# Kernel optimization log

Hardware: AMD Instinct MI355X
Metric: run time of the kernel (lower is better)

The kernel has to match this reference:

```python
import jax, jax.numpy as jnp
import numpy as np

N = 320          # number of valid codes in the batch
D = 128          # spatial dims; embeddings are (N, D+1) Lorentz points
MIN_DIST = 0.1
MARGIN = 0.1
WEIGHT = 0.1


def setup_inputs() -> dict:
    key = jax.random.key(0)
    k1, k2 = jax.random.split(key)
    # Valid hyperboloid points: x0 = sqrt(1 + ||x_spatial||^2)
    sp = 0.5 * jax.random.normal(k1, (N, D), dtype=jnp.float32)
    x0 = jnp.sqrt(1.0 + jnp.sum(sp * sp, axis=-1, keepdims=True))
    embeddings = jnp.concatenate([x0, sp], axis=-1)  # (N, D+1)
    # Symmetric nonnegative tree-distance matrix with zero diagonal
    td = jax.random.uniform(k2, (N, N), dtype=jnp.float32) * 8.0
    td = 0.5 * (td + td.T)
    td = td * (1.0 - jnp.eye(N, dtype=jnp.float32))
    return {"embeddings": embeddings, "tree_distances": td}


def _lorentz_pairwise(x):
    # Lorentz (hyperboloid) distance: d = arccosh(-<x,y>_L),
    # <x,y>_L = -x0*y0 + x_sp . y_sp
    t = x[:, :1]
    sp = x[:, 1:]
    inner = sp @ sp.T - t @ t.T  # (N, N) Minkowski inner product
    return jnp.arccosh(jnp.clip(-inner, 1.0 + 1e-7, None))


def reference(embeddings, tree_distances):
    emb = _lorentz_pairwise(embeddings)      # (N, N) embedding distances
    gt = tree_distances                       # (N, N) ground-truth distances
    n = gt.shape[0]
    # valid[a, j]: gt distance >= min_distance and j != a
    valid = (gt >= MIN_DIST) & (~jnp.eye(n, dtype=bool))
    # axes: (anchor a, j, k).  s > 0 iff gt[a,j] < gt[a,k]
    s = jnp.sign(gt[:, None, :] - gt[:, :, None])          # (N, N, N)
    diff = emb[:, :, None] - emb[:, None, :]                # e_j - e_k
    viol = jax.nn.relu(s * diff + MARGIN)                   # (N, N, N)
    tri = jnp.triu(jnp.ones((n, n), dtype=bool), 1)[None]   # j < k
    mask = valid[:, :, None] & valid[:, None, :] & tri & (s != 0.0)
    total = jnp.sum(jnp.where(mask, viol, 0.0))
    count = jnp.sum((viol > 0.0) & mask).astype(jnp.float32)
    return WEIGHT * jnp.where(count > 0.0, total / jnp.maximum(count, 1.0), 0.0)
```

## Files before the change

kernel.cpp:

```cpp
#include <hip/hip_runtime.h>
#include <math.h>

#define NN 320
#define DFULL 129
#define MIN_DIST_F 0.1f
#define MARGIN_F 0.1f
#define WEIGHT_F 0.1f
#define KG 5
#define JC 4
#define JLEN 80
#define NPART (NN*KG*JC)
#define NTILE 20
#define NTRI (NTILE*(NTILE+1)/2)

__device__ __forceinline__ int tri_off(int a) { return a * NTILE - (a * (a - 1)) / 2; }

__global__ __launch_bounds__(256) void lorentz_kernel(const float* __restrict__ E,
                                                      const float* __restrict__ gt,
                                                      float* __restrict__ embp) {
    const int t = blockIdx.x;
    float fa = (2.0f * NTILE + 1.0f - sqrtf((2.0f*NTILE+1.0f)*(2.0f*NTILE+1.0f) - 8.0f * (float)t)) * 0.5f;
    int a = (int)fa;
    if (a > 0 && tri_off(a) > t) --a;
    if (tri_off(a + 1) <= t) ++a;
    const int b = a + (t - tri_off(a));
    const int i0 = a * 16, j0 = b * 16;

    __shared__ float As[16][DFULL];
    __shared__ float Bs[16][DFULL];
    for (int q = threadIdx.x; q < 16 * DFULL; q += 256) {
        int r = q / DFULL, c = q - r * DFULL;
        As[r][c] = E[(i0 + r) * DFULL + c];
        Bs[r][c] = E[(j0 + r) * DFULL + c];
    }
    __syncthreads();
    const int ti = threadIdx.x & 15;
    const int tj = threadIdx.x >> 4;
    const int i = i0 + tj, j = j0 + ti;
    float tt = As[tj][0] * Bs[ti][0];
    float ss = 0.0f;
    #pragma unroll
    for (int d = 1; d < DFULL; ++d) ss = fmaf(As[tj][d], Bs[ti][d], ss);
    float x = fmaxf(tt - ss, 1.0f + 1e-7f);
    float e = acoshf(x);
    float g = gt[i * NN + j];
    float ep = (g >= MIN_DIST_F && i != j) ? e : __builtin_nanf("");
    embp[i * NN + j] = ep;
    embp[j * NN + i] = ep;
}

__global__ __launch_bounds__(64) void loss_kernel(const float* __restrict__ embp,
                                                  const float* __restrict__ gt,
                                                  float2* __restrict__ partial) {
    const int i    = blockIdx.x;
    const int kg   = blockIdx.y;
    const int jc   = blockIdx.z;
    const int lane = threadIdx.x;
    const int k    = kg * 64 + lane;

    const float* __restrict__ erow = embp + i * NN;
    const float* __restrict__ grow = gt   + i * NN;
    const float ek = erow[k];
    const float gk = grow[k];

    float tot = 0.0f, cnt = 0.0f;
    const int j0 = jc * JLEN;
    #pragma unroll
    for (int jb = 0; jb < JLEN; jb += 4) {
        const float4 e4 = *reinterpret_cast<const float4*>(erow + j0 + jb);
        const float4 g4 = *reinterpret_cast<const float4*>(grow + j0 + jb);
        {   float d = gk - g4.x; float v = fmaf(copysignf(1.0f, d), e4.x - ek, MARGIN_F);
            bool p = v > 0.0f; tot += p ? v : 0.0f; cnt += p ? 1.0f : 0.0f; }
        {   float d = gk - g4.y; float v = fmaf(copysignf(1.0f, d), e4.y - ek, MARGIN_F);
            bool p = v > 0.0f; tot += p ? v : 0.0f; cnt += p ? 1.0f : 0.0f; }
        {   float d = gk - g4.z; float v = fmaf(copysignf(1.0f, d), e4.z - ek, MARGIN_F);
            bool p = v > 0.0f; tot += p ? v : 0.0f; cnt += p ? 1.0f : 0.0f; }
        {   float d = gk - g4.w; float v = fmaf(copysignf(1.0f, d), e4.w - ek, MARGIN_F);
            bool p = v > 0.0f; tot += p ? v : 0.0f; cnt += p ? 1.0f : 0.0f; }
    }
    const bool self = (ek == ek) && (k >= j0) && (k < j0 + JLEN);
    if (self) { tot -= MARGIN_F; cnt -= 1.0f; }

    for (int off = 32; off > 0; off >>= 1) {
        tot += __shfl_down(tot, off, 64);
        cnt += __shfl_down(cnt, off, 64);
    }
    if (lane == 0) partial[(jc * KG + kg) * NN + i] = make_float2(tot, cnt);
}

__global__ __launch_bounds__(NN) void finalize_kernel(const float2* __restrict__ partial,
                                                      float* __restrict__ out) {
    const int t = threadIdx.x;
    float T = 0.0f, C = 0.0f;
    #pragma unroll
    for (int q = 0; q < NPART / NN; ++q) {
        float2 p = partial[q * NN + t];
        T += p.x; C += p.y;
    }
    for (int off = 32; off > 0; off >>= 1) {
        T += __shfl_down(T, off, 64);
        C += __shfl_down(C, off, 64);
    }
    __shared__ float wt[5], wc[5];
    const int lane = t & 63, wid = t >> 6;
    if (lane == 0) { wt[wid] = T; wc[wid] = C; }
    __syncthreads();
    if (t == 0) {
        float Tt = 0.0f, Ct = 0.0f;
        #pragma unroll
        for (int w = 0; w < 5; w++) { Tt += wt[w]; Ct += wc[w]; }
        out[0] = (Ct > 0.0f) ? WEIGHT_F * Tt / Ct : 0.0f;
    }
}

extern "C" void kernel_launch(void* const* d_in, const int* in_sizes, int n_in,
                              void* d_out, int out_size, void* d_ws, size_t ws_size,
                              hipStream_t stream) {
    const float* E  = (const float*)d_in[0];
    const float* gt = (const float*)d_in[1];
    float* out = (float*)d_out;
    float2* partial = (float2*)d_ws;
    float*  embp = (float*)((char*)d_ws + NPART * 8);

    lorentz_kernel<<<NTRI, 256, 0, stream>>>(E, gt, embp);
    dim3 g2(NN, KG, JC);
    loss_kernel<<<g2, 64, 0, stream>>>(embp, gt, partial);
    finalize_kernel<<<1, NN, 0, stream>>>(partial, out);
}
```

Baseline: 21.16 us.

## Fuse finalize into loss kernel via last-block atomic gate reduction

Removes the separate finalize launch. The loss kernel is now a persistent grid of 256 blocks that loop over the work units, and the last block to finish, found with an atomic counter reset by the lorentz kernel, reduces the per-block partials. Counts are accumulated as integers through ballot and popcount, and each block combines its waves' partials in shared memory. This saves one kernel launch and the many tiny 64-thread blocks, at the cost of atomics, fences and a serial tail in the last block.

Result: slower. 29.67 us (+40.2%).

```diff
diff --git a/kernel.cpp b/kernel.cpp
--- a/kernel.cpp
+++ b/kernel.cpp
@@ -6,18 +6,21 @@
 #define MIN_DIST_F 0.1f
 #define MARGIN_F 0.1f
 #define WEIGHT_F 0.1f
-#define KG 5
-#define JC 4
-#define JLEN 80
-#define NPART (NN*KG*JC)
 #define NTILE 20
 #define NTRI (NTILE*(NTILE+1)/2)
+#define JLEN 80
+#define NUNITS 6400
+#define LBLK 256
+#define LTHR 512
+#define NWAVE (LBLK*(LTHR/64))
 
 __device__ __forceinline__ int tri_off(int a) { return a * NTILE - (a * (a - 1)) / 2; }
 
 __global__ __launch_bounds__(256) void lorentz_kernel(const float* __restrict__ E,
                                                       const float* __restrict__ gt,
-                                                      float* __restrict__ embp) {
+                                                      float* __restrict__ embp,
+                                                      unsigned* __restrict__ gate) {
+    if (blockIdx.x == 0 && threadIdx.x == 0) *gate = 0u;
     const int t = blockIdx.x;
     float fa = (2.0f * NTILE + 1.0f - sqrtf((2.0f*NTILE+1.0f)*(2.0f*NTILE+1.0f) - 8.0f * (float)t)) * 0.5f;
     int a = (int)fa;
@@ -49,67 +52,89 @@
     embp[j * NN + i] = ep;
 }
 
-__global__ __launch_bounds__(64) void loss_kernel(const float* __restrict__ embp,
-                                                  const float* __restrict__ gt,
-                                                  float2* __restrict__ partial) {
-    const int i    = blockIdx.x;
-    const int kg   = blockIdx.y;
-    const int jc   = blockIdx.z;
-    const int lane = threadIdx.x;
-    const int k    = kg * 64 + lane;
+__global__ __launch_bounds__(LTHR) void loss_kernel(const float* __restrict__ embp,
+                                                    const float* __restrict__ gt,
+                                                    unsigned* __restrict__ gate,
+                                                    float* __restrict__ pT,
+                                                    float* __restrict__ pC,
+                                                    float* __restrict__ out) {
+    const int lane = threadIdx.x & 63;
+    const int wid  = threadIdx.x >> 6;
+    const int gw   = blockIdx.x * (LTHR / 64) + wid;
 
-    const float* __restrict__ erow = embp + i * NN;
-    const float* __restrict__ grow = gt   + i * NN;
-    const float ek = erow[k];
-    const float gk = grow[k];
+    float tot = 0.0f;
+    int   cnt = 0;
 
-    float tot = 0.0f, cnt = 0.0f;
-    const int j0 = jc * JLEN;
-    #pragma unroll
-    for (int jb = 0; jb < JLEN; jb += 4) {
-        const float4 e4 = *reinterpret_cast<const float4*>(erow + j0 + jb);
-        const float4 g4 = *reinterpret_cast<const float4*>(grow + j0 + jb);
-        {   float d = gk - g4.x; float v = fmaf(copysignf(1.0f, d), e4.x - ek, MARGIN_F);
-            bool p = v > 0.0f; tot += p ? v : 0.0f; cnt += p ? 1.0f : 0.0f; }
-        {   float d = gk - g4.y; float v = fmaf(copysignf(1.0f, d), e4.y - ek, MARGIN_F);
-            bool p = v > 0.0f; tot += p ? v : 0.0f; cnt += p ? 1.0f : 0.0f; }
-        {   float d = gk - g4.z; float v = fmaf(copysignf(1.0f, d), e4.z - ek, MARGIN_F);
-            bool p = v > 0.0f; tot += p ? v : 0.0f; cnt += p ? 1.0f : 0.0f; }
-        {   float d = gk - g4.w; float v = fmaf(copysignf(1.0f, d), e4.w - ek, MARGIN_F);
-            bool p = v > 0.0f; tot += p ? v : 0.0f; cnt += p ? 1.0f : 0.0f; }
+    for (int unit = gw; unit < NUNITS; unit += NWAVE) {
+        const int i  = unit / 20;
+        const int r  = unit - i * 20;
+        const int kg = r >> 2;
+        const int jc = r & 3;
+        const int k  = (kg << 6) + lane;
+        const float* __restrict__ erow = embp + i * NN;
+        const float* __restrict__ grow = gt   + i * NN;
+        const float ek = erow[k];
+        const float gk = grow[k];
+        const int j0 = jc * JLEN;
+
+        #pragma unroll 4
+        for (int jb = 0; jb < JLEN; jb += 4) {
+            const float4 e4 = *reinterpret_cast<const float4*>(erow + j0 + jb);
+            const float4 g4 = *reinterpret_cast<const float4*>(grow + j0 + jb);
+            {   float d = gk - g4.x; float v = fmaf(copysignf(1.0f, d), e4.x - ek, MARGIN_F);
+                bool p = v > 0.0f; tot += p ? v : 0.0f; cnt += (int)__popcll(__ballot(p)); }
+            {   float d = gk - g4.y; float v = fmaf(copysignf(1.0f, d), e4.y - ek, MARGIN_F);
+                bool p = v > 0.0f; tot += p ? v : 0.0f; cnt += (int)__popcll(__ballot(p)); }
+            {   float d = gk - g4.z; float v = fmaf(copysignf(1.0f, d), e4.z - ek, MARGIN_F);
+                bool p = v > 0.0f; tot += p ? v : 0.0f; cnt += (int)__popcll(__ballot(p)); }
+            {   float d = gk - g4.w; float v = fmaf(copysignf(1.0f, d), e4.w - ek, MARGIN_F);
+                bool p = v > 0.0f; tot += p ? v : 0.0f; cnt += (int)__popcll(__ballot(p)); }
+        }
+        bool self = (ek == ek) && (k >= j0) && (k < j0 + JLEN);
+        tot -= self ? MARGIN_F : 0.0f;
+        cnt -= (int)__popcll(__ballot(self));
     }
-    const bool self = (ek == ek) && (k >= j0) && (k < j0 + JLEN);
-    if (self) { tot -= MARGIN_F; cnt -= 1.0f; }
 
-    for (int off = 32; off > 0; off >>= 1) {
-        tot += __shfl_down(tot, off, 64);
-        cnt += __shfl_down(cnt, off, 64);
+    for (int off = 32; off > 0; off >>= 1) tot += __shfl_down(tot, off, 64);
+
+    __shared__ float wt[LTHR / 64];
+    __shared__ int   wc[LTHR / 64];
+    __shared__ int   sWinner;
+    if (lane == 0) { wt[wid] = tot; wc[wid] = cnt; }
+    __syncthreads();
+
+    if (threadIdx.x == 0) {
+        float T = 0.0f; int C = 0;
+        #pragma unroll
+        for (int w = 0; w < LTHR / 64; ++w) { T += wt[w]; C += wc[w]; }
+        atomicExch(&pT[blockIdx.x], T);
+        atomicExch(&pC[blockIdx.x], (float)C);
+        __threadfence();
+        unsigned old = atomicAdd(gate, 1u);
+        sWinner = (old == (unsigned)(LBLK - 1)) ? 1 : 0;
     }
-    if (lane == 0) partial[(jc * KG + kg) * NN + i] = make_float2(tot, cnt);
-}
+    __syncthreads();
 
-__global__ __launch_bounds__(NN) void finalize_kernel(const float2* __restrict__ partial,
-                                                      float* __restrict__ out) {
-    const int t = threadIdx.x;
-    float T = 0.0f, C = 0.0f;
-    #pragma unroll
-    for (int q = 0; q < NPART / NN; ++q) {
-        float2 p = partial[q * NN + t];
-        T += p.x; C += p.y;
-    }
-    for (int off = 32; off > 0; off >>= 1) {
-        T += __shfl_down(T, off, 64);
-        C += __shfl_down(C, off, 64);
-    }
-    __shared__ float wt[5], wc[5];
-    const int lane = t & 63, wid = t >> 6;
-    if (lane == 0) { wt[wid] = T; wc[wid] = C; }
-    __syncthreads();
-    if (t == 0) {
-        float Tt = 0.0f, Ct = 0.0f;
-        #pragma unroll
-        for (int w = 0; w < 5; w++) { Tt += wt[w]; Ct += wc[w]; }
-        out[0] = (Ct > 0.0f) ? WEIGHT_F * Tt / Ct : 0.0f;
+    if (sWinner) {
+        __threadfence();
+        float T = 0.0f, C = 0.0f;
+        if (threadIdx.x < LBLK) {
+            T = atomicAdd(&pT[threadIdx.x], 0.0f);
+            C = atomicAdd(&pC[threadIdx.x], 0.0f);
+        }
+        for (int off = 32; off > 0; off >>= 1) {
+            T += __shfl_down(T, off, 64);
+            C += __shfl_down(C, off, 64);
+        }
+        __shared__ float ft[LTHR / 64], fc[LTHR / 64];
+        if (lane == 0) { ft[wid] = T; fc[wid] = C; }
+        __syncthreads();
+        if (threadIdx.x == 0) {
+            float Tt = 0.0f, Ct = 0.0f;
+            #pragma unroll
+            for (int w = 0; w < LTHR / 64; ++w) { Tt += ft[w]; Ct += fc[w]; }
+            out[0] = (Ct > 0.0f) ? WEIGHT_F * Tt / Ct : 0.0f;
+        }
     }
 }
 
@@ -119,11 +144,11 @@
     const float* E  = (const float*)d_in[0];
     const float* gt = (const float*)d_in[1];
     float* out = (float*)d_out;
-    float2* partial = (float2*)d_ws;
-    float*  embp = (float*)((char*)d_ws + NPART * 8);
+    unsigned* gate = (unsigned*)d_ws;
+    float* pT = (float*)((char*)d_ws + 256);
+    float* pC = (float*)((char*)d_ws + 256 + LBLK * 4);
+    float* embp = (float*)((char*)d_ws + 4096);
 
-    lorentz_kernel<<<NTRI, 256, 0, stream>>>(E, gt, embp);
-    dim3 g2(NN, KG, JC);
-    loss_kernel<<<g2, 64, 0, stream>>>(embp, gt, partial);
-    finalize_kernel<<<1, NN, 0, stream>>>(partial, out);
+    lorentz_kernel<<<NTRI, 256, 0, stream>>>(E, gt, embp, gate);
+    loss_kernel<<<LBLK, LTHR, 0, stream>>>(embp, gt, gate, pT, pC, out);
 }
```
